# Performance work log

Hardware: AMD Instinct MI355X
Metric: run time of the kernel (lower is better)

The kernel has to match this reference:

```python
import jax, jax.numpy as jnp
import numpy as np

K = 9          # neighbors kept after dilation
DILATION = 2   # top-k runs with K*DILATION then strided slice
EPS = 1e-12    # F.normalize eps


def setup_inputs() -> dict:
    key = jax.random.key(0)
    # x: [B, C, N, 1] feature map over N points with C channels
    x = jax.random.normal(key, (2, 64, 8192, 1), dtype=jnp.float32)
    return {"x": x}


def reference(x):
    k_total = K * DILATION
    # L2-normalize along channel dim (F.normalize(x, p=2, dim=1))
    norm = jnp.sqrt(jnp.sum(x * x, axis=1, keepdims=True))
    xn = x / jnp.maximum(norm, EPS)
    # [B, C, N, 1] -> [B, N, C]
    pts = jnp.transpose(jnp.squeeze(xn, -1), (0, 2, 1))
    B, N, _ = pts.shape
    # pairwise squared distances: ||xi||^2 - 2 xi.xj + ||xj||^2  -> [B, N, N]
    sq = jnp.sum(pts * pts, axis=-1, keepdims=True)            # [B, N, 1]
    dist = sq - 2.0 * jnp.einsum('bnc,bmc->bnm', pts, pts) + jnp.swapaxes(sq, 1, 2)
    # k nearest = top-k of negated distance (matches torch.topk(-dist, k))
    _, nn_idx = jax.lax.top_k(-dist, k_total)                  # [B, N, k_total] int32
    center_idx = jnp.broadcast_to(jnp.arange(N, dtype=nn_idx.dtype)[None, :, None],
                                  (B, N, k_total))
    edge_index = jnp.stack([nn_idx, center_idx], axis=0)       # [2, B, N, k_total]
    # dilation (non-stochastic path): strided slice over neighbor dim
    return edge_index[:, :, :, ::DILATION]                     # [2, B, N, K]
```

## Files before the change

### kernel.cpp

```cpp
#include <hip/hip_runtime.h>


#define NPTS  8192
#define CHN   64
#define NB    2
#define KF    18
#define KC    8
#define KM    20
#define KOUT  9
#define NPART 4
#define TPB   32

typedef unsigned u32;
typedef unsigned short u16;
typedef unsigned long long u64;
typedef __attribute__((ext_vector_type(4))) unsigned u32x4;
typedef __attribute__((ext_vector_type(8))) short bf16x8;
typedef __attribute__((ext_vector_type(4))) float f32x4;

__device__ __forceinline__ u32 umin32(u32 a, u32 b) { return a < b ? a : b; }
__device__ __forceinline__ u32 umax32(u32 a, u32 b) { return a > b ? a : b; }

__device__ __forceinline__ void split4(float4 v, u32* h, u32* l) {
  const u32 b0 = __float_as_uint(v.x), b1 = __float_as_uint(v.y);
  const u32 b2 = __float_as_uint(v.z), b3 = __float_as_uint(v.w);
  const float l0 = v.x - __uint_as_float(b0 & 0xffff0000u);
  const float l1 = v.y - __uint_as_float(b1 & 0xffff0000u);
  const float l2 = v.z - __uint_as_float(b2 & 0xffff0000u);
  const float l3 = v.w - __uint_as_float(b3 & 0xffff0000u);
  h[0] = __builtin_amdgcn_perm(b1, b0, 0x07060302u);
  h[1] = __builtin_amdgcn_perm(b3, b2, 0x07060302u);
  l[0] = __builtin_amdgcn_perm(__float_as_uint(l1), __float_as_uint(l0), 0x07060302u);
  l[1] = __builtin_amdgcn_perm(__float_as_uint(l3), __float_as_uint(l2), 0x07060302u);
}

__device__ __forceinline__ u32 mono32(float f) {
  const u32 u = __float_as_uint(f);
  const u32 s = (u32)((int)u >> 31);
  return u ^ (s | 0x80000000u);
}

template <int KK>
__device__ __forceinline__ void insmm(u32 key, u32 (&d)[KK]) {
#pragma unroll
  for (int k = KK - 1; k >= 1; --k) d[k] = umax32(d[k - 1], umin32(d[k], key));
  d[0] = umin32(d[0], key);
}

template <int KK>
__device__ __forceinline__ void ins64(u64 key, u64 (&d)[KK]) {
  if (key < d[KK - 1]) {
#pragma unroll
    for (int k = KK - 1; k >= 1; --k) {
      const bool up = d[k - 1] > key;
      const bool here = (!up) && (d[k] > key);
      d[k] = up ? d[k - 1] : (here ? key : d[k]);
    }
    if (d[0] > key) d[0] = key;
  }
}

__global__ __launch_bounds__(128) void prep_kernel(
    const float* __restrict__ x, float* __restrict__ pts, float* __restrict__ sq) {
  const int b = blockIdx.x >> 6;
  const int n = ((blockIdx.x & 63) << 7) + threadIdx.x;
  const float* __restrict__ xb = x + (size_t)b * CHN * NPTS + n;
  float v[CHN];
  float ss = 0.f;
#pragma unroll
  for (int c = 0; c < CHN; ++c) {
    v[c] = xb[(size_t)c * NPTS];
    ss = __fadd_rn(ss, __fmul_rn(v[c], v[c]));
  }
  const float den = fmaxf(__fsqrt_rn(ss), 1e-12f);
#pragma unroll
  for (int c = 0; c < CHN; ++c) v[c] = __fdiv_rn(v[c], den);
  float r[8];
#pragma unroll
  for (int j = 0; j < 8; ++j) r[j] = __fmul_rn(v[j], v[j]);
#pragma unroll
  for (int blk = 1; blk < 8; ++blk)
#pragma unroll
    for (int j = 0; j < 8; ++j)
      r[j] = __fadd_rn(r[j], __fmul_rn(v[8 * blk + j], v[8 * blk + j]));
  const float t0 = __fadd_rn(r[0], r[1]);
  const float t1 = __fadd_rn(r[2], r[3]);
  const float t2 = __fadd_rn(r[4], r[5]);
  const float t3 = __fadd_rn(r[6], r[7]);
  sq[(b << 13) + n] = __fadd_rn(__fadd_rn(t0, t1), __fadd_rn(t2, t3));
  float4* dst = (float4*)(pts + (size_t)(b * NPTS + n) * CHN);
#pragma unroll
  for (int u = 0; u < 16; ++u)
    dst[u] = make_float4(v[4 * u], v[4 * u + 1], v[4 * u + 2], v[4 * u + 3]);
}

__global__ __launch_bounds__(256, 3) void knn_part_kernel(
    const float* __restrict__ pts, const float* __restrict__ sq,
    u16* __restrict__ cand) {
  __shared__ __align__(16) u32 pp[2][4096];
  __shared__ float sqp[2][64];

  const int tid = threadIdx.x;
  const int vb = ((blockIdx.x & 7) << 7) + (blockIdx.x >> 3);
  const int part = vb >> 8;
  const int w = vb & 255;
  const int b = w >> 7;
  const int qbase = (w & 127) << 6;
  const int t_lo = part << 5;
  const float* __restrict__ pb = pts + ((size_t)b << 19);
  const float* __restrict__ sqb = sq + (b << 13);

  const int sr = tid >> 2, ssub = tid & 3;
  const int lane = tid & 63, wid = tid >> 6;
  const int qoff = (wid & 1) << 5;
  const int moff = (wid >> 1) << 5;
  const int l15 = lane & 15;
  const int h4 = lane >> 4;
  const int sw = l15 & 7;

  {
    const float4* qsrc =
        (const float4*)(pb + ((size_t)(qbase + sr) << 6) + (ssub << 4));
    const float4* psrc =
        (const float4*)(pb + ((size_t)((t_lo << 6) + sr) << 6) + (ssub << 4));
    u32 qh[8], ql[8], ph[8], pl[8];
#pragma unroll
    for (int q = 0; q < 4; ++q) {
      float4 qv = qsrc[q];
      qv.x = -qv.x; qv.y = -qv.y; qv.z = -qv.z; qv.w = -qv.w;
      split4(qv, qh + 2 * q, ql + 2 * q);
      split4(psrc[q], ph + 2 * q, pl + 2 * q);
    }
    const int qa = sr * 32 + (((ssub << 1) ^ (sr & 7)) << 2);
    const int qb2 = sr * 32 + ((((ssub << 1) + 1) ^ (sr & 7)) << 2);
    *(u32x4*)(pp[1] + qa) = *(u32x4*)qh;
    *(u32x4*)(pp[1] + qb2) = *(u32x4*)(qh + 4);
    *(u32x4*)(pp[1] + 2048 + qa) = *(u32x4*)ql;
    *(u32x4*)(pp[1] + 2048 + qb2) = *(u32x4*)(ql + 4);
    *(u32x4*)(pp[0] + qa) = *(u32x4*)ph;
    *(u32x4*)(pp[0] + qb2) = *(u32x4*)(ph + 4);
    *(u32x4*)(pp[0] + 2048 + qa) = *(u32x4*)pl;
    *(u32x4*)(pp[0] + 2048 + qb2) = *(u32x4*)(pl + 4);
    if (tid < 64) sqp[0][tid] = (sqb[(t_lo << 6) + tid] + 2.f) * 0.5f;
  }
  __syncthreads();

  bf16x8 ah[2][2], al[2][2];
#pragma unroll
  for (int g = 0; g < 2; ++g)
#pragma unroll
    for (int s = 0; s < 2; ++s) {
      const int row = qoff + (g << 4) + l15;
      const int off = row * 32 + ((((s << 2) + h4) ^ sw) << 2);
      ah[g][s] = __builtin_bit_cast(bf16x8, *(const u32x4*)(pp[1] + off));
      al[g][s] = __builtin_bit_cast(bf16x8, *(const u32x4*)(pp[1] + 2048 + off));
    }
  __syncthreads();

  u32 d[2][4][KC];
#pragma unroll
  for (int g = 0; g < 2; ++g)
#pragma unroll
    for (int i = 0; i < 4; ++i)
#pragma unroll
      for (int k = 0; k < KC; ++k) d[g][i][k] = 0xffffffffu;

  for (int tau = 0; tau < TPB; ++tau) {
    const int cur = tau & 1;
    float4 st[4];
    float sqv = 0.f;
    const bool more = (tau + 1) < TPB;
    if (more) {
      const float4* nsrc = (const float4*)(
          pb + ((size_t)(t_lo + tau + 1) << 12) + (sr << 6) + (ssub << 4));
#pragma unroll
      for (int q = 0; q < 4; ++q) st[q] = nsrc[q];
      if (tid < 64) sqv = sqb[((t_lo + tau + 1) << 6) + tid];
    }
    const u32* ppc = pp[cur];
#pragma unroll
    for (int f = 0; f < 2; ++f) {
      const int m_l = moff + (f << 4) + l15;
      const float sqm = sqp[cur][m_l];
      f32x4 acc[2];
      acc[0] = (f32x4){sqm, sqm, sqm, sqm};
      acc[1] = acc[0];
#pragma unroll
      for (int s = 0; s < 2; ++s) {
        const u32* hb = ppc + m_l * 32 + ((((s << 2) + h4) ^ sw) << 2);
        const bf16x8 bh = __builtin_bit_cast(bf16x8, *(const u32x4*)hb);
        const bf16x8 bl = __builtin_bit_cast(bf16x8, *(const u32x4*)(hb + 2048));
        acc[0] = __builtin_amdgcn_mfma_f32_16x16x32_bf16(ah[0][s], bh, acc[0], 0, 0, 0);
        acc[1] = __builtin_amdgcn_mfma_f32_16x16x32_bf16(ah[1][s], bh, acc[1], 0, 0, 0);
        acc[0] = __builtin_amdgcn_mfma_f32_16x16x32_bf16(al[0][s], bh, acc[0], 0, 0, 0);
        acc[1] = __builtin_amdgcn_mfma_f32_16x16x32_bf16(al[1][s], bh, acc[1], 0, 0, 0);
        acc[0] = __builtin_amdgcn_mfma_f32_16x16x32_bf16(ah[0][s], bl, acc[0], 0, 0, 0);
        acc[1] = __builtin_amdgcn_mfma_f32_16x16x32_bf16(ah[1][s], bl, acc[1], 0, 0, 0);
      }
      const u32 lidx = (u32)((tau << 6) + m_l);
#pragma unroll
      for (int g = 0; g < 2; ++g)
#pragma unroll
        for (int i = 0; i < 4; ++i) {
          const u32 key = (__float_as_uint(acc[g][i]) & 0xfffff000u) | lidx;
          insmm<KC>(key, d[g][i]);
        }
    }
    if (more) {
      u32 hh[8], ll[8];
#pragma unroll
      for (int q = 0; q < 4; ++q) split4(st[q], hh + 2 * q, ll + 2 * q);
      u32* wp = pp[cur ^ 1];
      const int qa = sr * 32 + (((ssub << 1) ^ (sr & 7)) << 2);
      const int qb2 = sr * 32 + ((((ssub << 1) + 1) ^ (sr & 7)) << 2);
      *(u32x4*)(wp + qa) = *(u32x4*)hh;
      *(u32x4*)(wp + qb2) = *(u32x4*)(hh + 4);
      *(u32x4*)(wp + 2048 + qa) = *(u32x4*)ll;
      *(u32x4*)(wp + 2048 + qb2) = *(u32x4*)(ll + 4);
      if (tid < 64) sqp[cur ^ 1][tid] = (sqv + 2.f) * 0.5f;
    }
    __syncthreads();
  }

  u32* mg = &pp[0][0];
  const int stream = ((wid >> 1) << 4) + l15;
  const int rcb = ((wid & 1) << 4) + (h4 << 2);
#pragma unroll
  for (int chunk = 0; chunk < 2; ++chunk) {
#pragma unroll
    for (int i = 0; i < 4; ++i) {
      u32* wr = mg + ((rcb + i) * 32 + stream) * 8;
      u32x4 a, c;
      a.x = d[chunk][i][0]; a.y = d[chunk][i][1];
      a.z = d[chunk][i][2]; a.w = d[chunk][i][3];
      c.x = d[chunk][i][4]; c.y = d[chunk][i][5];
      c.z = d[chunk][i][6]; c.w = d[chunk][i][7];
      *(u32x4*)wr = a;
      *(u32x4*)(wr + 4) = c;
    }
    __syncthreads();
    {
      const int rowc = tid >> 3, oct = tid & 7;
      u32* base = mg + rowc * 256 + oct * 32;
      u32 m1[14];
#pragma unroll
      for (int k = 0; k < 14; ++k) m1[k] = 0xffffffffu;
#pragma unroll
      for (int j = 0; j < 8; ++j) {
        const u32x4 k4 = *(const u32x4*)(base + (j << 2));
        insmm<14>(k4.x, m1);
        insmm<14>(k4.y, m1);
        insmm<14>(k4.z, m1);
        insmm<14>(k4.w, m1);
      }
#pragma unroll
      for (int k = 0; k < 14; ++k) base[k] = m1[k];
    }
    __syncthreads();
    if (tid < 64) {
      const int rowc = tid >> 1, half = tid & 1;
      u32* rb = mg + rowc * 256 + half * 128;
      u32 m2[KM];
#pragma unroll
      for (int k = 0; k < KM; ++k) m2[k] = 0xffffffffu;
#pragma unroll
      for (int o = 0; o < 4; ++o) {
        const u32* p = rb + o * 32;
        for (int j = 0; j < 14; ++j) insmm<KM>(p[j], m2);
      }
#pragma unroll
      for (int k = 0; k < KM; ++k) rb[k] = m2[k];
    }
    __syncthreads();
    if (tid < 32) {
      u32 m3[KM];
#pragma unroll
      for (int k = 0; k < KM; ++k) m3[k] = 0xffffffffu;
      const u32* p0 = mg + tid * 256;
      for (int j = 0; j < KM; ++j) insmm<KM>(p0[j], m3);
      const u32* p1 = mg + tid * 256 + 128;
      for (int j = 0; j < KM; ++j) insmm<KM>(p1[j], m3);
      const int row = ((tid >> 4) << 5) + (chunk << 4) + (tid & 15);
      const int rg = (b << 13) + qbase + row;
      u16* cw = cand + (size_t)rg * (NPART * KM) + part * KM;
#pragma unroll
      for (int k = 0; k < KM; ++k)
        cw[k] = (u16)((part << 11) + (m3[k] & 0xfffu));
    }
    __syncthreads();
  }
}

__global__ __launch_bounds__(256) void finalize_kernel(
    const float* __restrict__ pts, const float* __restrict__ sq,
    const u16* __restrict__ cand, int* __restrict__ out) {
  __shared__ u64 ex[64 * 80];
  const int tid = threadIdx.x;
  const int rl = tid >> 2, sub = tid & 3;
  const int row = blockIdx.x * 64 + rl;
  const int b = row >> 13;
  const float* __restrict__ qrow = pts + ((size_t)row << 6);
  const float sqn = sq[row];
  const u16* __restrict__ cr = cand + (size_t)row * 80 + sub * 20;
  for (int j = 0; j < 20; ++j) {
    const int ix = cr[j];
    const float* __restrict__ pv = pts + ((size_t)((b << 13) + ix) << 6);
    float dot = 0.f;
#pragma unroll
    for (int c = 0; c < CHN; ++c)
      dot = __fadd_rn(dot, __fmul_rn(qrow[c], pv[c]));
    const float dist =
        __fadd_rn(__fsub_rn(sqn, __fmul_rn(2.0f, dot)), sq[(b << 13) + ix]);
    ex[rl * 80 + sub * 20 + j] = ((u64)mono32(dist) << 32) | (unsigned)ix;
  }
  __syncthreads();
  if (tid < 64) {
    u64 m18[KF];
#pragma unroll
    for (int k = 0; k < KF; ++k) m18[k] = ~0ull;
    for (int j = 0; j < 80; ++j) ins64<KF>(ex[tid * 80 + j], m18);
    const int row2 = blockIdx.x * 64 + tid;
    const int n2 = row2 & 8191;
    int* o0 = out + (size_t)row2 * KOUT;
    int* o1 = o0 + NB * NPTS * KOUT;
#pragma unroll
    for (int k = 0; k < KOUT; ++k) {
      o0[k] = (int)(m18[2 * k] & 0xffffffffu);
      o1[k] = n2;
    }
  }
}

extern "C" void kernel_launch(void* const* d_in, const int* in_sizes, int n_in,
                              void* d_out, int out_size, void* d_ws, size_t ws_size,
                              hipStream_t stream) {
  const float* x = (const float*)d_in[0];
  float* pts = (float*)d_ws;
  float* sqg = pts + (size_t)NB * NPTS * CHN;
  u16* cand = (u16*)(sqg + NB * NPTS);
  int* out = (int*)d_out;
  prep_kernel<<<dim3(128), dim3(128), 0, stream>>>(x, pts, sqg);
  knn_part_kernel<<<dim3(1024), dim3(256), 0, stream>>>(pts, sqg, cand);
  finalize_kernel<<<dim3(256), dim3(256), 0, stream>>>(pts, sqg, cand, out);
}
```

Measured before the change: 241.7 us.

## Precompute swizzled bf16 hi/lo split in prep and widen finalize parallelism

The prep kernel now writes pre-split bf16 hi/lo planes in the swizzled shared-memory layout. The kNN kernel can then copy tiles straight into LDS and read query fragments directly from global memory, with sign flips applied by XOR, so the per-tile split work disappears. A second prep kernel rewrites fp32 normalized points into the same workspace region after the kNN pass, adding an extra launch and a second read of the input. Finalize uses 512 threads and does a two-stage top-k merge to spread the sorting work.

```diff
diff --git a/kernel.cpp b/kernel.cpp
--- a/kernel.cpp
+++ b/kernel.cpp
@@ -21,19 +21,6 @@
 __device__ __forceinline__ u32 umin32(u32 a, u32 b) { return a < b ? a : b; }
 __device__ __forceinline__ u32 umax32(u32 a, u32 b) { return a > b ? a : b; }
 
-__device__ __forceinline__ void split4(float4 v, u32* h, u32* l) {
-  const u32 b0 = __float_as_uint(v.x), b1 = __float_as_uint(v.y);
-  const u32 b2 = __float_as_uint(v.z), b3 = __float_as_uint(v.w);
-  const float l0 = v.x - __uint_as_float(b0 & 0xffff0000u);
-  const float l1 = v.y - __uint_as_float(b1 & 0xffff0000u);
-  const float l2 = v.z - __uint_as_float(b2 & 0xffff0000u);
-  const float l3 = v.w - __uint_as_float(b3 & 0xffff0000u);
-  h[0] = __builtin_amdgcn_perm(b1, b0, 0x07060302u);
-  h[1] = __builtin_amdgcn_perm(b3, b2, 0x07060302u);
-  l[0] = __builtin_amdgcn_perm(__float_as_uint(l1), __float_as_uint(l0), 0x07060302u);
-  l[1] = __builtin_amdgcn_perm(__float_as_uint(l3), __float_as_uint(l2), 0x07060302u);
-}
-
 __device__ __forceinline__ u32 mono32(float f) {
   const u32 u = __float_as_uint(f);
   const u32 s = (u32)((int)u >> 31);
@@ -60,12 +47,8 @@
   }
 }
 
-__global__ __launch_bounds__(128) void prep_kernel(
-    const float* __restrict__ x, float* __restrict__ pts, float* __restrict__ sq) {
-  const int b = blockIdx.x >> 6;
-  const int n = ((blockIdx.x & 63) << 7) + threadIdx.x;
-  const float* __restrict__ xb = x + (size_t)b * CHN * NPTS + n;
-  float v[CHN];
+__device__ __forceinline__ void np_normalize(const float* __restrict__ xb,
+                                             float (&v)[CHN]) {
   float ss = 0.f;
 #pragma unroll
   for (int c = 0; c < CHN; ++c) {
@@ -75,6 +58,15 @@
   const float den = fmaxf(__fsqrt_rn(ss), 1e-12f);
 #pragma unroll
   for (int c = 0; c < CHN; ++c) v[c] = __fdiv_rn(v[c], den);
+}
+
+__global__ __launch_bounds__(128) void prep_kernel(
+    const float* __restrict__ x, u32* __restrict__ hib, u32* __restrict__ lob,
+    float* __restrict__ sq) {
+  const int b = blockIdx.x >> 6;
+  const int n = ((blockIdx.x & 63) << 7) + threadIdx.x;
+  float v[CHN];
+  np_normalize(x + (size_t)b * CHN * NPTS + n, v);
   float r[8];
 #pragma unroll
   for (int j = 0; j < 8; ++j) r[j] = __fmul_rn(v[j], v[j]);
@@ -88,6 +80,35 @@
   const float t2 = __fadd_rn(r[4], r[5]);
   const float t3 = __fadd_rn(r[6], r[7]);
   sq[(b << 13) + n] = __fadd_rn(__fadd_rn(t0, t1), __fadd_rn(t2, t3));
+  u32* hd = hib + (size_t)((b << 13) + n) * 32;
+  u32* ld = lob + (size_t)((b << 13) + n) * 32;
+  const int key = n & 7;
+#pragma unroll
+  for (int q = 0; q < 8; ++q) {
+    u32 h[4], l[4];
+#pragma unroll
+    for (int p2 = 0; p2 < 4; ++p2) {
+      const float a = v[8 * q + 2 * p2];
+      const float c = v[8 * q + 2 * p2 + 1];
+      const u32 ba = __float_as_uint(a), bc = __float_as_uint(c);
+      const float la = a - __uint_as_float(ba & 0xffff0000u);
+      const float lc = c - __uint_as_float(bc & 0xffff0000u);
+      h[p2] = __builtin_amdgcn_perm(bc, ba, 0x07060302u);
+      l[p2] = __builtin_amdgcn_perm(__float_as_uint(lc), __float_as_uint(la),
+                                    0x07060302u);
+    }
+    const int pq = (q ^ key) << 2;
+    *(u32x4*)(hd + pq) = (u32x4){h[0], h[1], h[2], h[3]};
+    *(u32x4*)(ld + pq) = (u32x4){l[0], l[1], l[2], l[3]};
+  }
+}
+
+__global__ __launch_bounds__(128) void prep2_kernel(
+    const float* __restrict__ x, float* __restrict__ pts) {
+  const int b = blockIdx.x >> 6;
+  const int n = ((blockIdx.x & 63) << 7) + threadIdx.x;
+  float v[CHN];
+  np_normalize(x + (size_t)b * CHN * NPTS + n, v);
   float4* dst = (float4*)(pts + (size_t)(b * NPTS + n) * CHN);
 #pragma unroll
   for (int u = 0; u < 16; ++u)
@@ -95,8 +116,8 @@
 }
 
 __global__ __launch_bounds__(256, 3) void knn_part_kernel(
-    const float* __restrict__ pts, const float* __restrict__ sq,
-    u16* __restrict__ cand) {
+    const u32* __restrict__ hib, const u32* __restrict__ lob,
+    const float* __restrict__ sq, u16* __restrict__ cand) {
   __shared__ __align__(16) u32 pp[2][4096];
   __shared__ float sqp[2][64];
 
@@ -107,10 +128,10 @@
   const int b = w >> 7;
   const int qbase = (w & 127) << 6;
   const int t_lo = part << 5;
-  const float* __restrict__ pb = pts + ((size_t)b << 19);
+  const u32* __restrict__ hb_ = hib + ((size_t)b << 18);
+  const u32* __restrict__ lb_ = lob + ((size_t)b << 18);
   const float* __restrict__ sqb = sq + (b << 13);
 
-  const int sr = tid >> 2, ssub = tid & 3;
   const int lane = tid & 63, wid = tid >> 6;
   const int qoff = (wid & 1) << 5;
   const int moff = (wid >> 1) << 5;
@@ -119,41 +140,30 @@
   const int sw = l15 & 7;
 
   {
-    const float4* qsrc =
-        (const float4*)(pb + ((size_t)(qbase + sr) << 6) + (ssub << 4));
-    const float4* psrc =
-        (const float4*)(pb + ((size_t)((t_lo << 6) + sr) << 6) + (ssub << 4));
-    u32 qh[8], ql[8], ph[8], pl[8];
-#pragma unroll
-    for (int q = 0; q < 4; ++q) {
-      float4 qv = qsrc[q];
-      qv.x = -qv.x; qv.y = -qv.y; qv.z = -qv.z; qv.w = -qv.w;
-      split4(qv, qh + 2 * q, ql + 2 * q);
-      split4(psrc[q], ph + 2 * q, pl + 2 * q);
-    }
-    const int qa = sr * 32 + (((ssub << 1) ^ (sr & 7)) << 2);
-    const int qb2 = sr * 32 + ((((ssub << 1) + 1) ^ (sr & 7)) << 2);
-    *(u32x4*)(pp[1] + qa) = *(u32x4*)qh;
-    *(u32x4*)(pp[1] + qb2) = *(u32x4*)(qh + 4);
-    *(u32x4*)(pp[1] + 2048 + qa) = *(u32x4*)ql;
-    *(u32x4*)(pp[1] + 2048 + qb2) = *(u32x4*)(ql + 4);
-    *(u32x4*)(pp[0] + qa) = *(u32x4*)ph;
-    *(u32x4*)(pp[0] + qb2) = *(u32x4*)(ph + 4);
-    *(u32x4*)(pp[0] + 2048 + qa) = *(u32x4*)pl;
-    *(u32x4*)(pp[0] + 2048 + qb2) = *(u32x4*)(pl + 4);
+    const u32* sH = hb_ + ((size_t)t_lo << 11);
+    const u32* sL = lb_ + ((size_t)t_lo << 11);
+    *(u32x4*)(pp[0] + (tid << 2)) = *(const u32x4*)(sH + (tid << 2));
+    *(u32x4*)(pp[0] + 1024 + (tid << 2)) = *(const u32x4*)(sH + 1024 + (tid << 2));
+    *(u32x4*)(pp[0] + 2048 + (tid << 2)) = *(const u32x4*)(sL + (tid << 2));
+    *(u32x4*)(pp[0] + 3072 + (tid << 2)) = *(const u32x4*)(sL + 1024 + (tid << 2));
     if (tid < 64) sqp[0][tid] = (sqb[(t_lo << 6) + tid] + 2.f) * 0.5f;
   }
-  __syncthreads();
 
   bf16x8 ah[2][2], al[2][2];
 #pragma unroll
   for (int g = 0; g < 2; ++g)
 #pragma unroll
     for (int s = 0; s < 2; ++s) {
-      const int row = qoff + (g << 4) + l15;
+      const int row = qbase + qoff + (g << 4) + l15;
       const int off = row * 32 + ((((s << 2) + h4) ^ sw) << 2);
-      ah[g][s] = __builtin_bit_cast(bf16x8, *(const u32x4*)(pp[1] + off));
-      al[g][s] = __builtin_bit_cast(bf16x8, *(const u32x4*)(pp[1] + 2048 + off));
+      u32x4 hv = *(const u32x4*)(hb_ + off);
+      u32x4 lv = *(const u32x4*)(lb_ + off);
+      hv.x ^= 0x80008000u; hv.y ^= 0x80008000u;
+      hv.z ^= 0x80008000u; hv.w ^= 0x80008000u;
+      lv.x ^= 0x80008000u; lv.y ^= 0x80008000u;
+      lv.z ^= 0x80008000u; lv.w ^= 0x80008000u;
+      ah[g][s] = __builtin_bit_cast(bf16x8, hv);
+      al[g][s] = __builtin_bit_cast(bf16x8, lv);
     }
   __syncthreads();
 
@@ -167,14 +177,16 @@
 
   for (int tau = 0; tau < TPB; ++tau) {
     const int cur = tau & 1;
-    float4 st[4];
+    u32x4 st[4];
     float sqv = 0.f;
     const bool more = (tau + 1) < TPB;
     if (more) {
-      const float4* nsrc = (const float4*)(
-          pb + ((size_t)(t_lo + tau + 1) << 12) + (sr << 6) + (ssub << 4));
-#pragma unroll
-      for (int q = 0; q < 4; ++q) st[q] = nsrc[q];
+      const u32* sH = hb_ + ((size_t)(t_lo + tau + 1) << 11);
+      const u32* sL = lb_ + ((size_t)(t_lo + tau + 1) << 11);
+      st[0] = *(const u32x4*)(sH + (tid << 2));
+      st[1] = *(const u32x4*)(sH + 1024 + (tid << 2));
+      st[2] = *(const u32x4*)(sL + (tid << 2));
+      st[3] = *(const u32x4*)(sL + 1024 + (tid << 2));
       if (tid < 64) sqv = sqb[((t_lo + tau + 1) << 6) + tid];
     }
     const u32* ppc = pp[cur];
@@ -187,9 +199,9 @@
       acc[1] = acc[0];
 #pragma unroll
       for (int s = 0; s < 2; ++s) {
-        const u32* hb = ppc + m_l * 32 + ((((s << 2) + h4) ^ sw) << 2);
-        const bf16x8 bh = __builtin_bit_cast(bf16x8, *(const u32x4*)hb);
-        const bf16x8 bl = __builtin_bit_cast(bf16x8, *(const u32x4*)(hb + 2048));
+        const u32* hp = ppc + m_l * 32 + ((((s << 2) + h4) ^ sw) << 2);
+        const bf16x8 bh = __builtin_bit_cast(bf16x8, *(const u32x4*)hp);
+        const bf16x8 bl = __builtin_bit_cast(bf16x8, *(const u32x4*)(hp + 2048));
         acc[0] = __builtin_amdgcn_mfma_f32_16x16x32_bf16(ah[0][s], bh, acc[0], 0, 0, 0);
         acc[1] = __builtin_amdgcn_mfma_f32_16x16x32_bf16(ah[1][s], bh, acc[1], 0, 0, 0);
         acc[0] = __builtin_amdgcn_mfma_f32_16x16x32_bf16(al[0][s], bh, acc[0], 0, 0, 0);
@@ -202,21 +214,16 @@
       for (int g = 0; g < 2; ++g)
 #pragma unroll
         for (int i = 0; i < 4; ++i) {
-          const u32 key = (__float_as_uint(acc[g][i]) & 0xfffff000u) | lidx;
-          insmm<KC>(key, d[g][i]);
+          const u32 keyv = (__float_as_uint(acc[g][i]) & 0xfffff000u) | lidx;
+          insmm<KC>(keyv, d[g][i]);
         }
     }
     if (more) {
-      u32 hh[8], ll[8];
-#pragma unroll
-      for (int q = 0; q < 4; ++q) split4(st[q], hh + 2 * q, ll + 2 * q);
       u32* wp = pp[cur ^ 1];
-      const int qa = sr * 32 + (((ssub << 1) ^ (sr & 7)) << 2);
-      const int qb2 = sr * 32 + ((((ssub << 1) + 1) ^ (sr & 7)) << 2);
-      *(u32x4*)(wp + qa) = *(u32x4*)hh;
-      *(u32x4*)(wp + qb2) = *(u32x4*)(hh + 4);
-      *(u32x4*)(wp + 2048 + qa) = *(u32x4*)ll;
-      *(u32x4*)(wp + 2048 + qb2) = *(u32x4*)(ll + 4);
+      *(u32x4*)(wp + (tid << 2)) = st[0];
+      *(u32x4*)(wp + 1024 + (tid << 2)) = st[1];
+      *(u32x4*)(wp + 2048 + (tid << 2)) = st[2];
+      *(u32x4*)(wp + 3072 + (tid << 2)) = st[3];
       if (tid < 64) sqp[cur ^ 1][tid] = (sqv + 2.f) * 0.5f;
     }
     __syncthreads();
@@ -291,18 +298,22 @@
   }
 }
 
-__global__ __launch_bounds__(256) void finalize_kernel(
+__global__ __launch_bounds__(512) void finalize_kernel(
     const float* __restrict__ pts, const float* __restrict__ sq,
     const u16* __restrict__ cand, int* __restrict__ out) {
-  __shared__ u64 ex[64 * 80];
+  __shared__ u64 ex[64 * 81];
+  __shared__ u64 hf[128 * 19];
   const int tid = threadIdx.x;
-  const int rl = tid >> 2, sub = tid & 3;
-  const int row = blockIdx.x * 64 + rl;
+  const int rl = tid >> 3, sub = tid & 7;
+  const int row = (blockIdx.x << 6) + rl;
   const int b = row >> 13;
+  const float sqn = sq[row];
   const float* __restrict__ qrow = pts + ((size_t)row << 6);
-  const float sqn = sq[row];
-  const u16* __restrict__ cr = cand + (size_t)row * 80 + sub * 20;
-  for (int j = 0; j < 20; ++j) {
+  const float* __restrict__ sqb = sq + (b << 13);
+  const u16* __restrict__ cr = cand + (size_t)row * 80 + sub * 10;
+  u64* exw = ex + rl * 81 + sub * 10;
+#pragma unroll 2
+  for (int j = 0; j < 10; ++j) {
     const int ix = cr[j];
     const float* __restrict__ pv = pts + ((size_t)((b << 13) + ix) << 6);
     float dot = 0.f;
@@ -310,23 +321,37 @@
     for (int c = 0; c < CHN; ++c)
       dot = __fadd_rn(dot, __fmul_rn(qrow[c], pv[c]));
     const float dist =
-        __fadd_rn(__fsub_rn(sqn, __fmul_rn(2.0f, dot)), sq[(b << 13) + ix]);
-    ex[rl * 80 + sub * 20 + j] = ((u64)mono32(dist) << 32) | (unsigned)ix;
+        __fadd_rn(__fsub_rn(sqn, __fmul_rn(2.0f, dot)), sqb[ix]);
+    exw[j] = ((u64)mono32(dist) << 32) | (u32)ix;
+  }
+  __syncthreads();
+  if (tid < 128) {
+    const int r2 = tid >> 1, hv = tid & 1;
+    u64 m18[KF];
+#pragma unroll
+    for (int k = 0; k < KF; ++k) m18[k] = ~0ull;
+    const u64* p = ex + r2 * 81 + hv * 40;
+    for (int j = 0; j < 40; ++j) ins64<KF>(p[j], m18);
+    u64* wr = hf + tid * 19;
+#pragma unroll
+    for (int k = 0; k < KF; ++k) wr[k] = m18[k];
   }
   __syncthreads();
   if (tid < 64) {
     u64 m18[KF];
 #pragma unroll
     for (int k = 0; k < KF; ++k) m18[k] = ~0ull;
-    for (int j = 0; j < 80; ++j) ins64<KF>(ex[tid * 80 + j], m18);
-    const int row2 = blockIdx.x * 64 + tid;
-    const int n2 = row2 & 8191;
+    const u64* p0 = hf + (tid << 1) * 19;
+    const u64* p1 = hf + ((tid << 1) + 1) * 19;
+    for (int j = 0; j < KF; ++j) ins64<KF>(p0[j], m18);
+    for (int j = 0; j < KF; ++j) ins64<KF>(p1[j], m18);
+    const int row2 = (blockIdx.x << 6) + tid;
     int* o0 = out + (size_t)row2 * KOUT;
     int* o1 = o0 + NB * NPTS * KOUT;
 #pragma unroll
     for (int k = 0; k < KOUT; ++k) {
       o0[k] = (int)(m18[2 * k] & 0xffffffffu);
-      o1[k] = n2;
+      o1[k] = row2 & 8191;
     }
   }
 }
@@ -335,11 +360,14 @@
                               void* d_out, int out_size, void* d_ws, size_t ws_size,
                               hipStream_t stream) {
   const float* x = (const float*)d_in[0];
+  u32* hib = (u32*)d_ws;
+  u32* lob = hib + (size_t)NB * NPTS * 32;
   float* pts = (float*)d_ws;
-  float* sqg = pts + (size_t)NB * NPTS * CHN;
+  float* sqg = (float*)(hib + (size_t)NB * NPTS * 64);
   u16* cand = (u16*)(sqg + NB * NPTS);
   int* out = (int*)d_out;
-  prep_kernel<<<dim3(128), dim3(128), 0, stream>>>(x, pts, sqg);
-  knn_part_kernel<<<dim3(1024), dim3(256), 0, stream>>>(pts, sqg, cand);
-  finalize_kernel<<<dim3(256), dim3(256), 0, stream>>>(pts, sqg, cand, out);
-}
+  prep_kernel<<<dim3(128), dim3(128), 0, stream>>>(x, hib, lob, sqg);
+  knn_part_kernel<<<dim3(1024), dim3(256), 0, stream>>>(hib, lob, sqg, cand);
+  prep2_kernel<<<dim3(128), dim3(128), 0, stream>>>(x, pts);
+  finalize_kernel<<<dim3(256), dim3(512), 0, stream>>>(pts, sqg, cand, out);
+}
```

New measurement: 261.3 us. +8.1%, slower.
